# Kernel tuning notes

Measured on AMD Instinct MI355X. Metric: run time of the kernel, lower is better.

## Reference

```python
import jax, jax.numpy as jnp
import numpy as np
import math

POOL = 7          # RoIAlign output_size
SR = 2            # sampling_ratio


def _roi_align(feat, boxes, bidx):
    """torchvision RoIAlign, aligned=False, spatial_scale=1.0, sampling_ratio=2.
    feat: [B,C,H,W]; boxes: [N,4] (x1,y1,x2,y2) in pixel coords of this level;
    bidx: [N] int batch indices. Returns [N,C,POOL,POOL]."""
    B, C, H, W = feat.shape
    x1, y1, x2, y2 = boxes[:, 0], boxes[:, 1], boxes[:, 2], boxes[:, 3]
    roi_w = jnp.maximum(x2 - x1, 1.0)
    roi_h = jnp.maximum(y2 - y1, 1.0)
    bin_w = roi_w / POOL
    bin_h = roi_h / POOL
    # sample-point offsets within the ROI, in bin units: [POOL, SR]
    off = jnp.arange(POOL, dtype=feat.dtype)[:, None] + (jnp.arange(SR, dtype=feat.dtype)[None, :] + 0.5) / SR
    ys = y1[:, None, None] + bin_h[:, None, None] * off  # [N,POOL,SR]
    xs = x1[:, None, None] + bin_w[:, None, None] * off  # [N,POOL,SR]

    def prep(c, size):
        valid = (c > -1.0) & (c < size)
        c = jnp.clip(c, 0.0, size - 1)
        lo = jnp.floor(c).astype(jnp.int32)
        hi = jnp.minimum(lo + 1, size - 1)
        return lo, hi, c - lo, valid

    y_lo, y_hi, fy, vy = prep(ys, H)
    x_lo, x_hi, fx, vx = prep(xs, W)

    b = bidx.astype(jnp.int32)[:, None, None, None, None]  # [N,1,1,1,1]

    def gather(yi, xi):
        # -> [N,POOL,SR,POOL,SR,C] (advanced indices broadcast, channel slice last)
        return feat[b, :, yi[:, :, :, None, None], xi[:, None, None, :, :]]

    hy = (1.0 - fy)[:, :, :, None, None, None]
    ly = fy[:, :, :, None, None, None]
    hx = (1.0 - fx)[:, None, None, :, :, None]
    lx = fx[:, None, None, :, :, None]
    v = (gather(y_lo, x_lo) * hy * hx + gather(y_lo, x_hi) * hy * lx
         + gather(y_hi, x_lo) * ly * hx + gather(y_hi, x_hi) * ly * lx)
    valid = (vy[:, :, :, None, None] & vx[:, None, None, :, :])[..., None]
    v = jnp.where(valid, v, 0.0)
    out = v.mean(axis=(2, 4))          # average over SRxSR samples -> [N,POOL,POOL,C]
    return out.transpose(0, 3, 1, 2)   # [N,C,POOL,POOL]


def setup_inputs() -> dict:
    key = jax.random.key(0)
    k2, k3, k4, k5, kxy, kwh, kbi = jax.random.split(key, 7)
    N = 1000
    p2 = jax.random.normal(k2, (2, 256, 256, 256), dtype=jnp.float32)
    p3 = jax.random.normal(k3, (2, 256, 128, 128), dtype=jnp.float32)
    p4 = jax.random.normal(k4, (2, 256, 64, 64), dtype=jnp.float32)
    p5 = jax.random.normal(k5, (2, 256, 32, 32), dtype=jnp.float32)
    xy = jax.random.uniform(kxy, (N, 2), minval=0.0, maxval=0.7)
    wh = jax.random.uniform(kwh, (N, 2), minval=0.02, maxval=0.3)
    rpn_bbox = jnp.concatenate([xy, xy + wh], axis=1)  # (x1,y1,x2,y2) normalized
    box_index = jax.random.randint(kbi, (N,), 0, 2, dtype=jnp.int32)
    return {"p2": p2, "p3": p3, "p4": p4, "p5": p5,
            "rpn_bbox": rpn_bbox, "box_index": box_index}


def reference(p2, p3, p4, p5, rpn_bbox, box_index):
    feats = [p2, p3, p4, p5]
    N = rpn_bbox.shape[0]
    x1, y1, x2, y2 = rpn_bbox[:, 0], rpn_bbox[:, 1], rpn_bbox[:, 2], rpn_bbox[:, 3]
    area = (y2 - y1) * (x2 - x1)
    roi_level = jnp.log(jnp.sqrt(area)) / math.log(2.0)
    roi_level = jnp.clip(jnp.round(roi_level) + 4.0, 0.0, 3.0).astype(jnp.int32)
    # Compute RoIAlign of every ROI at every level, then select per-ROI level.
    # (The masked-select / per-level dispatch / argsort-combine in the original
    # restores original ROI order, so this is mathematically identical.)
    pooled_per_level = jnp.stack(
        [_roi_align(f, rpn_bbox * f.shape[3], box_index) for f in feats], axis=0
    )  # [4, N, C, 7, 7]
    pooled = pooled_per_level[roi_level, jnp.arange(N)]  # [N, C, 7, 7]
    return pooled
```

## Files before the change

### kernel.cpp

```cpp
#include <hip/hip_runtime.h>
#include <math.h>

#define POOL 7
#define NCELL 49
#define NCH 256
#define CH_SPLIT 8
#define CHPB (NCH / CH_SPLIT)
#define CHPW (CHPB / 4)
#define LDSF 640
#define NIT_S 10
#define NBUCK 512

typedef float f32x2 __attribute__((ext_vector_type(2)));

typedef __attribute__((address_space(1))) void global_void;
typedef __attribute__((address_space(3))) void lds_void;
__device__ __forceinline__ void stage4(const float* g, float* l) {
    __builtin_amdgcn_global_load_lds((global_void*)g, (lds_void*)l, 4, 0, 0);
}
__device__ __forceinline__ void stage16(const float* g, float* l) {
    __builtin_amdgcn_global_load_lds((global_void*)g, (lds_void*)l, 16, 0, 0);
}
__device__ __forceinline__ unsigned ldsaddr(const float* p) {
    return (unsigned)(uintptr_t)(lds_void*)(void*)const_cast<float*>(p);
}

template <int V> __device__ __forceinline__ void vwait() {
    if constexpr (V == 0)  asm volatile("s_waitcnt vmcnt(0)" ::: "memory");
    else if constexpr (V == 1)  asm volatile("s_waitcnt vmcnt(1)" ::: "memory");
    else if constexpr (V == 2)  asm volatile("s_waitcnt vmcnt(2)" ::: "memory");
    else if constexpr (V == 3)  asm volatile("s_waitcnt vmcnt(3)" ::: "memory");
    else if constexpr (V == 4)  asm volatile("s_waitcnt vmcnt(4)" ::: "memory");
    else if constexpr (V == 6)  asm volatile("s_waitcnt vmcnt(6)" ::: "memory");
    else if constexpr (V == 10) asm volatile("s_waitcnt vmcnt(10)" ::: "memory");
    else if constexpr (V == 20) asm volatile("s_waitcnt vmcnt(20)" ::: "memory");
}

struct Tab {
    int loff0[4], loff1[4];
    float w00[4], w01[4], w10[4], w11[4];
};

__device__ __forceinline__ void make_tab(Tab& tb, int lane, int W, int rs, int xb, int y0,
                                         float x1, float y1, float bin_w, float bin_h)
{
    int cell = (lane < NCELL) ? lane : (NCELL - 1);
    int py = cell / POOL, px = cell % POOL;
#pragma unroll
    for (int s = 0; s < 4; ++s) {
        int sy = s >> 1, sx = s & 1;
        float y = y1 + bin_h * ((float)py + ((float)sy + 0.5f) * 0.5f);
        float x = x1 + bin_w * ((float)px + ((float)sx + 0.5f) * 0.5f);
        bool v = (y > -1.f) && (y < (float)W) && (x > -1.f) && (x < (float)W);
        float yc = fminf(fmaxf(y, 0.f), (float)(W - 1));
        float xc = fminf(fmaxf(x, 0.f), (float)(W - 1));
        int ylo = (int)floorf(yc), xlo = (int)floorf(xc);
        int yhi = min(ylo + 1, W - 1);
        float fy = yc - (float)ylo, fx = xc - (float)xlo;
        float vv = v ? 0.25f : 0.f;
        int bxp = min(xlo, W - 2);
        bool in = (xlo == bxp);
        float wx0 = in ? (1.f - fx) : 0.f;
        float wx1 = in ? fx : 1.f;
        float wr0 = (1.f - fy) * vv, wr1 = fy * vv;
        tb.loff0[s] = (ylo - y0) * rs + (bxp - xb);
        tb.loff1[s] = (yhi - y0) * rs + (bxp - xb);
        tb.w00[s] = wr0 * wx0; tb.w01[s] = wr0 * wx1;
        tb.w10[s] = wr1 * wx0; tb.w11[s] = wr1 * wx1;
    }
}

__device__ __forceinline__ float consume(const float* cb, const Tab& tb)
{
    unsigned base = ldsaddr(cb);
    f32x2 p0[4], p1[4];
#pragma unroll
    for (int s = 0; s < 4; ++s) {
        unsigned a0 = base + 4u * (unsigned)tb.loff0[s];
        unsigned a1 = base + 4u * (unsigned)tb.loff1[s];
        asm volatile("ds_read2_b32 %0, %1 offset0:0 offset1:1" : "=v"(p0[s]) : "v"(a0));
        asm volatile("ds_read2_b32 %0, %1 offset0:0 offset1:1" : "=v"(p1[s]) : "v"(a1));
    }
    asm volatile("s_waitcnt lgkmcnt(0)" ::: "memory");
    __builtin_amdgcn_sched_barrier(0);
    float acc = 0.f;
#pragma unroll
    for (int s = 0; s < 4; ++s) {
        acc += tb.w00[s] * p0[s].x + tb.w01[s] * p0[s].y
             + tb.w10[s] * p1[s].x + tb.w11[s] * p1[s].y;
    }
    return acc;
}

template <int NIT4>
__device__ __forceinline__ void box_x4(
    const float* fbase, float* outp, float* sm, int lane,
    int W, int HW, int wwa, int y0, int x0a, int ngrp,
    float x1, float y1, float bin_w, float bin_h)
{
    int g_off[NIT4];
    bool act[NIT4];
    int wwa4 = wwa >> 2;
#pragma unroll
    for (int k = 0; k < NIT4; ++k) {
        int idx = k * 64 + lane;
        act[k] = idx < ngrp;
        int ii = act[k] ? idx : 0;
        int r = ii / wwa4;
        int c = ii - r * wwa4;
        g_off[k] = (y0 + r) * W + x0a + c * 4;
    }
#pragma unroll
    for (int k = 0; k < NIT4; ++k)
        if (act[k]) stage16(fbase + g_off[k], sm + k * 256);
#pragma unroll
    for (int k = 0; k < NIT4; ++k)
        if (act[k]) stage16(fbase + (size_t)HW + g_off[k], sm + LDSF + k * 256);

    Tab tb;
    make_tab(tb, lane, W, wwa, x0a, y0, x1, y1, bin_w, bin_h);

#pragma unroll
    for (int i = 0; i < CHPW; ++i) {
        if (i + 2 < CHPW) {
            const float* fc = fbase + (size_t)(i + 2) * HW;
            float* nb = sm + ((i + 2) % 3) * LDSF;
#pragma unroll
            for (int k = 0; k < NIT4; ++k)
                if (act[k]) stage16(fc + g_off[k], nb + k * 256);
            vwait<2 * NIT4>();
        } else if (i + 1 < CHPW) {
            vwait<NIT4>();
        } else {
            vwait<1>();
        }
        float acc = consume(sm + (i % 3) * LDSF, tb);
        if (lane < NCELL)
            __builtin_nontemporal_store(acc, outp + (size_t)i * NCELL);
    }
}

__device__ __forceinline__ void box_s(
    const float* fbase, float* outp, float* sm, int lane,
    int W, int HW, int ww, int y0, int x0, int packed,
    float x1, float y1, float bin_w, float bin_h)
{
    int g_off[NIT_S];
#pragma unroll
    for (int k = 0; k < NIT_S; ++k) {
        int idx = k * 64 + lane;
        idx = (idx < packed) ? idx : 0;
        int r = idx / ww;
        int c = idx - r * ww;
        g_off[k] = (y0 + r) * W + (x0 + c);
    }
#pragma unroll
    for (int k = 0; k < NIT_S; ++k) stage4(fbase + g_off[k], sm + k * 64);
#pragma unroll
    for (int k = 0; k < NIT_S; ++k) stage4(fbase + (size_t)HW + g_off[k], sm + LDSF + k * 64);

    Tab tb;
    make_tab(tb, lane, W, ww, x0, y0, x1, y1, bin_w, bin_h);

#pragma unroll
    for (int i = 0; i < CHPW; ++i) {
        if (i + 2 < CHPW) {
            const float* fc = fbase + (size_t)(i + 2) * HW;
            float* nb = sm + ((i + 2) % 3) * LDSF;
#pragma unroll
            for (int k = 0; k < NIT_S; ++k) stage4(fc + g_off[k], nb + k * 64);
            vwait<20>();
        } else if (i + 1 < CHPW) {
            vwait<10>();
        } else {
            vwait<1>();
        }
        float acc = consume(sm + (i % 3) * LDSF, tb);
        if (lane < NCELL)
            __builtin_nontemporal_store(acc, outp + (size_t)i * NCELL);
    }
}

__device__ __forceinline__ int box_key(const float* boxes, const int* bidx, int n)
{
    float bx1 = boxes[4 * n + 0], by1 = boxes[4 * n + 1];
    float bx2 = boxes[4 * n + 2], by2 = boxes[4 * n + 3];
    float area = (by2 - by1) * (bx2 - bx1);
    float lvlf = logf(sqrtf(area)) * 1.4426950408889634f;
    int level = (int)fminf(fmaxf(rintf(lvlf) + 4.0f, 0.0f), 3.0f);
    int b = bidx[n] & 1;
    float cx = 0.5f * (bx1 + bx2), cy = 0.5f * (by1 + by2);
    int qx = min(7, max(0, (int)(cx * 8.0f)));
    int qy = min(7, max(0, (int)(cy * 8.0f)));
    return (((((level << 1) | b) << 3) | qy) << 3) | qx;
}

__global__ __launch_bounds__(NBUCK) void box_sort_kernel(
    const float* __restrict__ boxes, const int* __restrict__ bidx,
    int* __restrict__ perm, int N)
{
    __shared__ int h0[NBUCK], h1[NBUCK];
    const int t = threadIdx.x;
    h0[t] = 0;
    __syncthreads();
    for (int n = t; n < N; n += NBUCK)
        atomicAdd(&h0[box_key(boxes, bidx, n)], 1);
    __syncthreads();
    int* src = h0; int* dst = h1;
    for (int off = 1; off < NBUCK; off <<= 1) {
        dst[t] = src[t] + ((t >= off) ? src[t - off] : 0);
        __syncthreads();
        int* tmp = src; src = dst; dst = tmp;
    }
    dst[t] = (t == 0) ? 0 : src[t - 1];
    __syncthreads();
    for (int n = t; n < N; n += NBUCK) {
        int slot = atomicAdd(&dst[box_key(boxes, bidx, n)], 1);
        perm[slot] = n;
    }
}

__global__ __launch_bounds__(256, 5) void roi_align_fpn_kernel(
    const float* __restrict__ p2, const float* __restrict__ p3,
    const float* __restrict__ p4, const float* __restrict__ p5,
    const float* __restrict__ boxes, const int* __restrict__ bidx,
    const int* __restrict__ perm,
    float* __restrict__ out, int N)
{
    __shared__ float smem[4][3][LDSF];
    const int n = perm ? perm[blockIdx.y] : (int)blockIdx.y;
    const int t = threadIdx.x;
    const int wave = t >> 6;
    const int lane = t & 63;

    float bx1 = boxes[4 * n + 0], by1 = boxes[4 * n + 1];
    float bx2 = boxes[4 * n + 2], by2 = boxes[4 * n + 3];
    float area = (by2 - by1) * (bx2 - bx1);
    float lvlf = logf(sqrtf(area)) * 1.4426950408889634f;
    int level = (int)fminf(fmaxf(rintf(lvlf) + 4.0f, 0.0f), 3.0f);
    int W = 256 >> level;
    int HW = W * W;
    float scale = (float)W;
    float x1 = bx1 * scale, y1 = by1 * scale;
    float bin_w = fmaxf((bx2 - bx1) * scale, 1.0f) * (1.0f / POOL);
    float bin_h = fmaxf((by2 - by1) * scale, 1.0f) * (1.0f / POOL);

    const float* feat = (level == 0) ? p2 : (level == 1) ? p3 : (level == 2) ? p4 : p5;
    feat += (size_t)bidx[n] * NCH * HW;

    float yA = y1 + bin_h * 0.25f, yB = y1 + bin_h * 6.75f;
    float xA = x1 + bin_w * 0.25f, xB = x1 + bin_w * 6.75f;
    int y0  = (int)floorf(fminf(fmaxf(yA, 0.f), (float)(W - 1)));
    int y1h = min((int)floorf(fminf(fmaxf(yB, 0.f), (float)(W - 1))) + 1, W - 1);
    int x0  = (int)floorf(fminf(fmaxf(xA, 0.f), (float)(W - 1)));
    x0 = min(x0, W - 2);
    int x1p = min((int)floorf(fminf(fmaxf(xB, 0.f), (float)(W - 1))) + 1, W - 1);
    int ww = x1p - x0 + 1;
    int wh = y1h - y0 + 1;

    int x0a = x0 & ~3;
    int wwa = ((x1p - x0a + 1) + 3) & ~3;
    if ((wwa & 7) == 0 && (wwa + 4) * wh <= LDSF) wwa += 4;
    int padded = wwa * wh;

    const int ch0 = blockIdx.x * CHPB + wave * CHPW;
    const float* fbase = feat + (size_t)ch0 * HW;
    float* sm = &smem[wave][0][0];
    int cell = (lane < NCELL) ? lane : (NCELL - 1);
    float* outp = out + (size_t)n * NCH * NCELL + (size_t)ch0 * NCELL + cell;

    if (padded <= LDSF) {
        int ngrp = (wwa >> 2) * wh;
        int nit4 = (ngrp + 63) >> 6;
        if (nit4 == 1)      box_x4<1>(fbase, outp, sm, lane, W, HW, wwa, y0, x0a, ngrp, x1, y1, bin_w, bin_h);
        else if (nit4 == 2) box_x4<2>(fbase, outp, sm, lane, W, HW, wwa, y0, x0a, ngrp, x1, y1, bin_w, bin_h);
        else                box_x4<3>(fbase, outp, sm, lane, W, HW, wwa, y0, x0a, ngrp, x1, y1, bin_w, bin_h);
    } else {
        int whc = min(wh, LDSF / ww);
        int packed = ww * whc;
        box_s(fbase, outp, sm, lane, W, HW, ww, y0, x0, packed, x1, y1, bin_w, bin_h);
    }
}

extern "C" void kernel_launch(void* const* d_in, const int* in_sizes, int n_in,
                              void* d_out, int out_size, void* d_ws, size_t ws_size,
                              hipStream_t stream) {
    const float* p2    = (const float*)d_in[0];
    const float* p3    = (const float*)d_in[1];
    const float* p4    = (const float*)d_in[2];
    const float* p5    = (const float*)d_in[3];
    const float* boxes = (const float*)d_in[4];
    const int*   bidx  = (const int*)d_in[5];
    float* out = (float*)d_out;
    int N = in_sizes[5];
    int* perm = nullptr;
    if (d_ws && ws_size >= (size_t)N * sizeof(int)) {
        perm = (int*)d_ws;
        box_sort_kernel<<<1, NBUCK, 0, stream>>>(boxes, bidx, perm, N);
    }
    dim3 grid(CH_SPLIT, N);
    roi_align_fpn_kernel<<<grid, 256, 0, stream>>>(p2, p3, p4, p5, boxes, bidx, perm, out, N);
}
```

Baseline: 266.1 us.

## Restructure channel pipeline into double-buffered channel pairs

```diff
diff --git a/kernel.cpp b/kernel.cpp
--- a/kernel.cpp
+++ b/kernel.cpp
@@ -27,13 +27,12 @@
 
 template <int V> __device__ __forceinline__ void vwait() {
     if constexpr (V == 0)  asm volatile("s_waitcnt vmcnt(0)" ::: "memory");
-    else if constexpr (V == 1)  asm volatile("s_waitcnt vmcnt(1)" ::: "memory");
     else if constexpr (V == 2)  asm volatile("s_waitcnt vmcnt(2)" ::: "memory");
-    else if constexpr (V == 3)  asm volatile("s_waitcnt vmcnt(3)" ::: "memory");
     else if constexpr (V == 4)  asm volatile("s_waitcnt vmcnt(4)" ::: "memory");
     else if constexpr (V == 6)  asm volatile("s_waitcnt vmcnt(6)" ::: "memory");
-    else if constexpr (V == 10) asm volatile("s_waitcnt vmcnt(10)" ::: "memory");
+    else if constexpr (V == 8)  asm volatile("s_waitcnt vmcnt(8)" ::: "memory");
     else if constexpr (V == 20) asm volatile("s_waitcnt vmcnt(20)" ::: "memory");
+    else if constexpr (V == 22) asm volatile("s_waitcnt vmcnt(22)" ::: "memory");
 }
 
 struct Tab {
@@ -110,34 +109,36 @@
         int c = ii - r * wwa4;
         g_off[k] = (y0 + r) * W + x0a + c * 4;
     }
-#pragma unroll
-    for (int k = 0; k < NIT4; ++k)
-        if (act[k]) stage16(fbase + g_off[k], sm + k * 256);
-#pragma unroll
-    for (int k = 0; k < NIT4; ++k)
-        if (act[k]) stage16(fbase + (size_t)HW + g_off[k], sm + LDSF + k * 256);
+    float* const buf0 = sm;
+    float* const buf1 = sm + 2 * LDSF;
+
+    auto do_stage = [&](int pair, float* buf) {
+#pragma unroll
+        for (int c = 0; c < 2; ++c) {
+            const float* fc = fbase + (size_t)(2 * pair + c) * HW;
+            float* nb = buf + c * LDSF;
+#pragma unroll
+            for (int k = 0; k < NIT4; ++k)
+                if (act[k]) stage16(fc + g_off[k], nb + k * 256);
+        }
+    };
+
+    do_stage(0, buf0);
 
     Tab tb;
     make_tab(tb, lane, W, wwa, x0a, y0, x1, y1, bin_w, bin_h);
 
-#pragma unroll
-    for (int i = 0; i < CHPW; ++i) {
-        if (i + 2 < CHPW) {
-            const float* fc = fbase + (size_t)(i + 2) * HW;
-            float* nb = sm + ((i + 2) % 3) * LDSF;
-#pragma unroll
-            for (int k = 0; k < NIT4; ++k)
-                if (act[k]) stage16(fc + g_off[k], nb + k * 256);
-            vwait<2 * NIT4>();
-        } else if (i + 1 < CHPW) {
-            vwait<NIT4>();
-        } else {
-            vwait<1>();
-        }
-        float acc = consume(sm + (i % 3) * LDSF, tb);
-        if (lane < NCELL)
-            __builtin_nontemporal_store(acc, outp + (size_t)i * NCELL);
-    }
+    auto do_cons = [&](int pair, const float* buf) {
+        float a0 = consume(buf, tb);
+        if (lane < NCELL) outp[(size_t)(2 * pair) * NCELL] = a0;
+        float a1 = consume(buf + LDSF, tb);
+        if (lane < NCELL) outp[(size_t)(2 * pair + 1) * NCELL] = a1;
+    };
+
+    do_stage(1, buf1);  vwait<2 * NIT4>();      do_cons(0, buf0);
+    do_stage(2, buf0);  vwait<2 * NIT4 + 2>();  do_cons(1, buf1);
+    do_stage(3, buf1);  vwait<2 * NIT4 + 2>();  do_cons(2, buf0);
+                        vwait<2>();             do_cons(3, buf1);
 }
 
 __device__ __forceinline__ void box_s(
@@ -154,31 +155,35 @@
         int c = idx - r * ww;
         g_off[k] = (y0 + r) * W + (x0 + c);
     }
-#pragma unroll
-    for (int k = 0; k < NIT_S; ++k) stage4(fbase + g_off[k], sm + k * 64);
-#pragma unroll
-    for (int k = 0; k < NIT_S; ++k) stage4(fbase + (size_t)HW + g_off[k], sm + LDSF + k * 64);
+    float* const buf0 = sm;
+    float* const buf1 = sm + 2 * LDSF;
+
+    auto do_stage = [&](int pair, float* buf) {
+#pragma unroll
+        for (int c = 0; c < 2; ++c) {
+            const float* fc = fbase + (size_t)(2 * pair + c) * HW;
+            float* nb = buf + c * LDSF;
+#pragma unroll
+            for (int k = 0; k < NIT_S; ++k) stage4(fc + g_off[k], nb + k * 64);
+        }
+    };
+
+    do_stage(0, buf0);
 
     Tab tb;
     make_tab(tb, lane, W, ww, x0, y0, x1, y1, bin_w, bin_h);
 
-#pragma unroll
-    for (int i = 0; i < CHPW; ++i) {
-        if (i + 2 < CHPW) {
-            const float* fc = fbase + (size_t)(i + 2) * HW;
-            float* nb = sm + ((i + 2) % 3) * LDSF;
-#pragma unroll
-            for (int k = 0; k < NIT_S; ++k) stage4(fc + g_off[k], nb + k * 64);
-            vwait<20>();
-        } else if (i + 1 < CHPW) {
-            vwait<10>();
-        } else {
-            vwait<1>();
-        }
-        float acc = consume(sm + (i % 3) * LDSF, tb);
-        if (lane < NCELL)
-            __builtin_nontemporal_store(acc, outp + (size_t)i * NCELL);
-    }
+    auto do_cons = [&](int pair, const float* buf) {
+        float a0 = consume(buf, tb);
+        if (lane < NCELL) outp[(size_t)(2 * pair) * NCELL] = a0;
+        float a1 = consume(buf + LDSF, tb);
+        if (lane < NCELL) outp[(size_t)(2 * pair + 1) * NCELL] = a1;
+    };
+
+    do_stage(1, buf1);  vwait<20>();  do_cons(0, buf0);
+    do_stage(2, buf0);  vwait<22>();  do_cons(1, buf1);
+    do_stage(3, buf1);  vwait<22>();  do_cons(2, buf0);
+                        vwait<2>();   do_cons(3, buf1);
 }
 
 __device__ __forceinline__ int box_key(const float* boxes, const int* bidx, int n)
@@ -220,14 +225,14 @@
     }
 }
 
-__global__ __launch_bounds__(256, 5) void roi_align_fpn_kernel(
+__global__ __launch_bounds__(256, 4) void roi_align_fpn_kernel(
     const float* __restrict__ p2, const float* __restrict__ p3,
     const float* __restrict__ p4, const float* __restrict__ p5,
     const float* __restrict__ boxes, const int* __restrict__ bidx,
     const int* __restrict__ perm,
     float* __restrict__ out, int N)
 {
-    __shared__ float smem[4][3][LDSF];
+    __shared__ float smem[4][2][2 * LDSF];
     const int n = perm ? perm[blockIdx.y] : (int)blockIdx.y;
     const int t = threadIdx.x;
     const int wave = t >> 6;
```

Result: no change. 261.9 us (-1.6%).

## Double channel split and stage all per-wave channels into LDS up front

Applied to the files above, without the earlier changes.

```diff
diff --git a/kernel.cpp b/kernel.cpp
--- a/kernel.cpp
+++ b/kernel.cpp
@@ -4,7 +4,7 @@
 #define POOL 7
 #define NCELL 49
 #define NCH 256
-#define CH_SPLIT 8
+#define CH_SPLIT 16
 #define CHPB (NCH / CH_SPLIT)
 #define CHPW (CHPB / 4)
 #define LDSF 640
@@ -26,14 +26,18 @@
 }
 
 template <int V> __device__ __forceinline__ void vwait() {
-    if constexpr (V == 0)  asm volatile("s_waitcnt vmcnt(0)" ::: "memory");
+    if constexpr (V == 0)       asm volatile("s_waitcnt vmcnt(0)" ::: "memory");
     else if constexpr (V == 1)  asm volatile("s_waitcnt vmcnt(1)" ::: "memory");
     else if constexpr (V == 2)  asm volatile("s_waitcnt vmcnt(2)" ::: "memory");
     else if constexpr (V == 3)  asm volatile("s_waitcnt vmcnt(3)" ::: "memory");
     else if constexpr (V == 4)  asm volatile("s_waitcnt vmcnt(4)" ::: "memory");
+    else if constexpr (V == 5)  asm volatile("s_waitcnt vmcnt(5)" ::: "memory");
     else if constexpr (V == 6)  asm volatile("s_waitcnt vmcnt(6)" ::: "memory");
-    else if constexpr (V == 10) asm volatile("s_waitcnt vmcnt(10)" ::: "memory");
-    else if constexpr (V == 20) asm volatile("s_waitcnt vmcnt(20)" ::: "memory");
+    else if constexpr (V == 7)  asm volatile("s_waitcnt vmcnt(7)" ::: "memory");
+    else if constexpr (V == 9)  asm volatile("s_waitcnt vmcnt(9)" ::: "memory");
+    else if constexpr (V == 12) asm volatile("s_waitcnt vmcnt(12)" ::: "memory");
+    else if constexpr (V == 21) asm volatile("s_waitcnt vmcnt(21)" ::: "memory");
+    else if constexpr (V == 30) asm volatile("s_waitcnt vmcnt(30)" ::: "memory");
 }
 
 struct Tab {
@@ -111,33 +115,25 @@
         g_off[k] = (y0 + r) * W + x0a + c * 4;
     }
 #pragma unroll
-    for (int k = 0; k < NIT4; ++k)
-        if (act[k]) stage16(fbase + g_off[k], sm + k * 256);
-#pragma unroll
-    for (int k = 0; k < NIT4; ++k)
-        if (act[k]) stage16(fbase + (size_t)HW + g_off[k], sm + LDSF + k * 256);
+    for (int c = 0; c < CHPW; ++c) {
+        const float* fc = fbase + (size_t)c * HW;
+        float* nb = sm + c * LDSF;
+#pragma unroll
+        for (int k = 0; k < NIT4; ++k)
+            if (act[k]) stage16(fc + g_off[k], nb + k * 256);
+    }
 
     Tab tb;
     make_tab(tb, lane, W, wwa, x0a, y0, x1, y1, bin_w, bin_h);
 
-#pragma unroll
-    for (int i = 0; i < CHPW; ++i) {
-        if (i + 2 < CHPW) {
-            const float* fc = fbase + (size_t)(i + 2) * HW;
-            float* nb = sm + ((i + 2) % 3) * LDSF;
-#pragma unroll
-            for (int k = 0; k < NIT4; ++k)
-                if (act[k]) stage16(fc + g_off[k], nb + k * 256);
-            vwait<2 * NIT4>();
-        } else if (i + 1 < CHPW) {
-            vwait<NIT4>();
-        } else {
-            vwait<1>();
-        }
-        float acc = consume(sm + (i % 3) * LDSF, tb);
-        if (lane < NCELL)
-            __builtin_nontemporal_store(acc, outp + (size_t)i * NCELL);
-    }
+    vwait<3 * NIT4>();
+    { float a = consume(sm, tb);            if (lane < NCELL) outp[0]                   = a; }
+    vwait<2 * NIT4 + 1>();
+    { float a = consume(sm + LDSF, tb);     if (lane < NCELL) outp[(size_t)NCELL]       = a; }
+    vwait<NIT4 + 2>();
+    { float a = consume(sm + 2 * LDSF, tb); if (lane < NCELL) outp[(size_t)(2 * NCELL)] = a; }
+    vwait<3>();
+    { float a = consume(sm + 3 * LDSF, tb); if (lane < NCELL) outp[(size_t)(3 * NCELL)] = a; }
 }
 
 __device__ __forceinline__ void box_s(
@@ -155,30 +151,24 @@
         g_off[k] = (y0 + r) * W + (x0 + c);
     }
 #pragma unroll
-    for (int k = 0; k < NIT_S; ++k) stage4(fbase + g_off[k], sm + k * 64);
-#pragma unroll
-    for (int k = 0; k < NIT_S; ++k) stage4(fbase + (size_t)HW + g_off[k], sm + LDSF + k * 64);
+    for (int c = 0; c < CHPW; ++c) {
+        const float* fc = fbase + (size_t)c * HW;
+        float* nb = sm + c * LDSF;
+#pragma unroll
+        for (int k = 0; k < NIT_S; ++k) stage4(fc + g_off[k], nb + k * 64);
+    }
 
     Tab tb;
     make_tab(tb, lane, W, ww, x0, y0, x1, y1, bin_w, bin_h);
 
-#pragma unroll
-    for (int i = 0; i < CHPW; ++i) {
-        if (i + 2 < CHPW) {
-            const float* fc = fbase + (size_t)(i + 2) * HW;
-            float* nb = sm + ((i + 2) % 3) * LDSF;
-#pragma unroll
-            for (int k = 0; k < NIT_S; ++k) stage4(fc + g_off[k], nb + k * 64);
-            vwait<20>();
-        } else if (i + 1 < CHPW) {
-            vwait<10>();
-        } else {
-            vwait<1>();
-        }
-        float acc = consume(sm + (i % 3) * LDSF, tb);
-        if (lane < NCELL)
-            __builtin_nontemporal_store(acc, outp + (size_t)i * NCELL);
-    }
+    vwait<30>();
+    { float a = consume(sm, tb);            if (lane < NCELL) outp[0]                   = a; }
+    vwait<21>();
+    { float a = consume(sm + LDSF, tb);     if (lane < NCELL) outp[(size_t)NCELL]       = a; }
+    vwait<12>();
+    { float a = consume(sm + 2 * LDSF, tb); if (lane < NCELL) outp[(size_t)(2 * NCELL)] = a; }
+    vwait<3>();
+    { float a = consume(sm + 3 * LDSF, tb); if (lane < NCELL) outp[(size_t)(3 * NCELL)] = a; }
 }
 
 __device__ __forceinline__ int box_key(const float* boxes, const int* bidx, int n)
@@ -220,14 +210,14 @@
     }
 }
 
-__global__ __launch_bounds__(256, 5) void roi_align_fpn_kernel(
+__global__ __launch_bounds__(256, 4) void roi_align_fpn_kernel(
     const float* __restrict__ p2, const float* __restrict__ p3,
     const float* __restrict__ p4, const float* __restrict__ p5,
     const float* __restrict__ boxes, const int* __restrict__ bidx,
     const int* __restrict__ perm,
     float* __restrict__ out, int N)
 {
-    __shared__ float smem[4][3][LDSF];
+    __shared__ float smem[4][CHPW][LDSF];
     const int n = perm ? perm[blockIdx.y] : (int)blockIdx.y;
     const int t = threadIdx.x;
     const int wave = t >> 6;
```

New measurement: 262.6 us. About the same (-1.3%).
